# Kernel tuning notes

Hardware: AMD Instinct MI355X
Metric: run time of the kernel (lower is better)

Reference implementation:

```python
import jax, jax.numpy as jnp
import numpy as np

IN_F = 1024
OUT_F = 1024
GRID = 8
TOKENS = 8192


def setup_inputs() -> dict:
    key = jax.random.key(0)
    k_x, k_w, k_b, k_s = jax.random.split(key, 4)
    x = jax.random.normal(k_x, (TOKENS, IN_F), dtype=jnp.float32)
    # kaiming_uniform_(nonlinearity='linear'): bound = sqrt(3/fan_in)
    bound_w = float(np.sqrt(3.0 / IN_F))
    W = jax.random.uniform(k_w, (OUT_F, IN_F), minval=-bound_w, maxval=bound_w, dtype=jnp.float32)
    # nn.Linear default bias init: U(-1/sqrt(fan_in), 1/sqrt(fan_in))
    bound_b = float(1.0 / np.sqrt(IN_F))
    b = jax.random.uniform(k_b, (OUT_F,), minval=-bound_b, maxval=bound_b, dtype=jnp.float32)
    spline_weight = jax.random.uniform(k_s, (OUT_F, IN_F, GRID), minval=-0.1, maxval=0.1, dtype=jnp.float32)
    grid = jnp.linspace(-3.0, 3.0, GRID, dtype=jnp.float32)
    return {"x": x, "W": W, "b": b, "spline_weight": spline_weight, "grid": grid}


def reference(x, W, b, spline_weight, grid):
    grid_size = spline_weight.shape[-1]
    # base path: Linear(silu(x))
    base = jnp.einsum('ti,oi->to', jax.nn.silu(x), W) + b
    # RBF basis: [tokens, in_features, grid_size]
    denom = 2.0 / (grid_size - 1) + 1e-05
    basis = jnp.exp(-(((x[..., None] - grid) / denom) ** 2))
    spline = jnp.einsum('tig,oig->to', basis, spline_weight)
    return base + spline
```

## Files before the change

kernel.cpp:

```cpp
#include <hip/hip_runtime.h>
#include <hip/hip_bf16.h>

#define IN_F   1024
#define OUT_F  1024
#define TOKENS 8192
#define KTOT   9216
#define KHALF  4608
#define NTILE  72

typedef __attribute__((ext_vector_type(8))) short  bf16x8;
typedef __attribute__((ext_vector_type(8))) unsigned short ushortx8;
typedef __attribute__((ext_vector_type(4))) float  f32x4;

template<int M> struct ModeT { static constexpr int value = M; };

__device__ __forceinline__ unsigned int f2bf(float f) {
    union { float f; unsigned int u; } v; v.f = f;
    unsigned int r = v.u + 0x7fffu + ((v.u >> 16) & 1u);
    return r >> 16;
}

__device__ __forceinline__ float bf2f(unsigned short h) {
    union { unsigned int u; float f; } v; v.u = ((unsigned int)h) << 16;
    return v.f;
}

__device__ __forceinline__ void prep_a_body(int idx, const float* __restrict__ x,
                                            const float* __restrict__ grid,
                                            unsigned short* __restrict__ A)
{
    int t = idx >> 10;
    int i = idx & 1023;
    float xv = x[idx];
    float sil = xv / (1.0f + __expf(-xv));
    A[(size_t)t * KTOT + i] = (unsigned short)f2bf(sil);

    const float invd = 1.0f / (2.0f / 7.0f + 1e-5f);
    unsigned int h[8];
    #pragma unroll
    for (int g = 0; g < 8; ++g) {
        float d = (xv - grid[g]) * invd;
        h[g] = f2bf(__expf(-d * d));
    }
    uint4 pk;
    pk.x = h[0] | (h[1] << 16);
    pk.y = h[2] | (h[3] << 16);
    pk.z = h[4] | (h[5] << 16);
    pk.w = h[6] | (h[7] << 16);
    *reinterpret_cast<uint4*>(&A[(size_t)t * KTOT + IN_F + (size_t)i * 8]) = pk;
}

__device__ __forceinline__ void prep_b_body(int idx, const float* __restrict__ W,
                                            const float* __restrict__ spl,
                                            unsigned short* __restrict__ B)
{
    int o  = idx / (KTOT / 8);
    int c8 = idx - o * (KTOT / 8);
    const float* src = (c8 < IN_F / 8)
        ? (W   + (size_t)o * IN_F     + (size_t)c8 * 8)
        : (spl + (size_t)o * IN_F * 8 + (size_t)(c8 - IN_F / 8) * 8);
    const float4* s4 = reinterpret_cast<const float4*>(src);
    float4 lo = s4[0], hi = s4[1];
    uint4 pk;
    pk.x = f2bf(lo.x) | (f2bf(lo.y) << 16);
    pk.y = f2bf(lo.z) | (f2bf(lo.w) << 16);
    pk.z = f2bf(hi.x) | (f2bf(hi.y) << 16);
    pk.w = f2bf(hi.z) | (f2bf(hi.w) << 16);
    *reinterpret_cast<uint4*>(&B[(size_t)o * KTOT + (size_t)c8 * 8]) = pk;
}

__global__ __launch_bounds__(256)
void prep_fused(const float* __restrict__ x, const float* __restrict__ grid,
                const float* __restrict__ W, const float* __restrict__ spl,
                unsigned short* __restrict__ A, unsigned short* __restrict__ B)
{
    int b = blockIdx.x;
    if (b < (TOKENS * IN_F) / 256)
        prep_a_body(b * 256 + threadIdx.x, x, grid, A);
    else
        prep_b_body((b - (TOKENS * IN_F) / 256) * 256 + threadIdx.x, W, spl, B);
}

__global__ __launch_bounds__(256)
void prep_a_kernel(const float* __restrict__ x, const float* __restrict__ grid,
                   unsigned short* __restrict__ A)
{
    prep_a_body(blockIdx.x * blockDim.x + threadIdx.x, x, grid, A);
}

__global__ __launch_bounds__(256)
void prep_b_kernel(const float* __restrict__ W, const float* __restrict__ spl,
                   unsigned short* __restrict__ B)
{
    prep_b_body(blockIdx.x * blockDim.x + threadIdx.x, W, spl, B);
}

#define GLOAD(src, dst) __builtin_amdgcn_global_load_lds( \
    (const __attribute__((address_space(1))) void*)(src),  \
    (__attribute__((address_space(3))) void*)(dst), 16, 0, 0)
#define SBAR()  __builtin_amdgcn_s_barrier()
#define SCH0()  __builtin_amdgcn_sched_barrier(0)
#define VMC0()  asm volatile("s_waitcnt vmcnt(0)" ::: "memory")

__global__ __launch_bounds__(512, 2)
void gemm_kan2(const unsigned short* __restrict__ A,
               const unsigned short* __restrict__ B,
               unsigned short* __restrict__ P, int rows)
{
    __shared__ char lds[131072];

    const int bid  = blockIdx.x;
    const int xcd  = bid & 7;
    const int j    = bid >> 3;
    const int sk   = j & 1;
    const int bn   = (j >> 1) & 3;
    const int bm   = (j >> 3) * 8 + xcd;
    const int tid  = threadIdx.x;
    const int wave = tid >> 6, lane = tid & 63;
    const int wr   = wave >> 2, wc = wave & 3;
    const int fr   = lane & 15, kg = lane >> 4;
    const int sw   = fr & 7;
    const int koff[2] = { (kg ^ sw) * 16, ((4 | kg) ^ sw) * 16 };
    const int k0 = sk * KHALF;

    const int trow = tid >> 3;
    const int ksrc = ((tid & 7) ^ (trow & 7)) * 8;
    const unsigned short* gA = A + (size_t)(bm * 256 + trow) * KTOT + k0 + ksrc;
    const unsigned short* gB = B + (size_t)(bn * 256 + trow) * KTOT + k0 + ksrc;
    const size_t R64 = (size_t)64 * KTOT;

    f32x4 acc[8][4];
    const f32x4 zero = {0.f, 0.f, 0.f, 0.f};
    #pragma unroll
    for (int m = 0; m < 8; ++m)
        #pragma unroll
        for (int n = 0; n < 4; ++n) acc[m][n] = zero;

    {
        char* dA = lds + tid * 16;
        char* dB = lds + 65536 + tid * 16;
        GLOAD(gA,           dA);           GLOAD(gA + R64,     dA + 8192);
        GLOAD(gA + 2 * R64, dA + 16384);   GLOAD(gA + 3 * R64, dA + 24576);
        GLOAD(gB,           dB);           GLOAD(gB + R64,     dB + 8192);
        GLOAD(gB + 2 * R64, dB + 16384);   GLOAD(gB + 3 * R64, dB + 24576);
        gA += 64; gB += 64;
    }
    VMC0(); SBAR(); SCH0();

    const int aOff = (wr * 64 + fr) * 128;
    const int bOff = (wc * 32 + fr) * 128;

    bf16x8 af[4][2], bfLo[2][2], bfHi[2][2];
    int u = 0;

    auto tile = [&](auto mC) {
        constexpr int MODE = decltype(mC)::value;
        char* bufA = lds + (u & 1) * 32768;
        char* bufB = lds + 65536 + (u & 1) * 32768;

        #pragma unroll
        for (int mi = 0; mi < 4; ++mi)
            #pragma unroll
            for (int ks = 0; ks < 2; ++ks)
                af[mi][ks] = *(const bf16x8*)(bufA + aOff + mi * 2048 + koff[ks]);
        #pragma unroll
        for (int ni = 0; ni < 2; ++ni)
            #pragma unroll
            for (int ks = 0; ks < 2; ++ks) {
                bfLo[ni][ks] = *(const bf16x8*)(bufB + bOff + ni * 2048 + koff[ks]);
                bfHi[ni][ks] = *(const bf16x8*)(bufB + bOff + 16384 + ni * 2048 + koff[ks]);
            }

        if constexpr (MODE == 0) {
            char* dA = lds + ((u & 1) ^ 1) * 32768 + tid * 16;
            char* dB = lds + 65536 + ((u & 1) ^ 1) * 32768 + tid * 16;
            GLOAD(gA,           dA);           GLOAD(gA + R64,     dA + 8192);
            GLOAD(gA + 2 * R64, dA + 16384);   GLOAD(gA + 3 * R64, dA + 24576);
            GLOAD(gB,           dB);           GLOAD(gB + R64,     dB + 8192);
            GLOAD(gB + 2 * R64, dB + 16384);   GLOAD(gB + 3 * R64, dB + 24576);
            gA += 64; gB += 64;
        }
        SCH0();

        __builtin_amdgcn_s_setprio(1);
        #pragma unroll
        for (int mi = 0; mi < 4; ++mi)
            #pragma unroll
            for (int ni = 0; ni < 2; ++ni)
                #pragma unroll
                for (int ks = 0; ks < 2; ++ks)
                    acc[mi][ni] = __builtin_amdgcn_mfma_f32_16x16x32_bf16(
                        af[mi][ks], bfLo[ni][ks], acc[mi][ni], 0, 0, 0);
        __builtin_amdgcn_s_setprio(0);

        __builtin_amdgcn_s_setprio(1);
        #pragma unroll
        for (int mi = 0; mi < 4; ++mi)
            #pragma unroll
            for (int ni = 0; ni < 2; ++ni)
                #pragma unroll
                for (int ks = 0; ks < 2; ++ks)
                    acc[mi][2 + ni] = __builtin_amdgcn_mfma_f32_16x16x32_bf16(
                        af[mi][ks], bfHi[ni][ks], acc[mi][2 + ni], 0, 0, 0);
        __builtin_amdgcn_s_setprio(0);

        #pragma unroll
        for (int mi = 0; mi < 4; ++mi)
            #pragma unroll
            for (int ks = 0; ks < 2; ++ks)
                af[mi][ks] = *(const bf16x8*)(bufA + aOff + 16384 + mi * 2048 + koff[ks]);

        __builtin_amdgcn_s_setprio(1);
        #pragma unroll
        for (int mi = 0; mi < 4; ++mi)
            #pragma unroll
            for (int ni = 0; ni < 2; ++ni)
                #pragma unroll
                for (int ks = 0; ks < 2; ++ks)
                    acc[4 + mi][ni] = __builtin_amdgcn_mfma_f32_16x16x32_bf16(
                        af[mi][ks], bfLo[ni][ks], acc[4 + mi][ni], 0, 0, 0);
        __builtin_amdgcn_s_setprio(0);

        __builtin_amdgcn_s_setprio(1);
        #pragma unroll
        for (int mi = 0; mi < 4; ++mi)
            #pragma unroll
            for (int ni = 0; ni < 2; ++ni)
                #pragma unroll
                for (int ks = 0; ks < 2; ++ks)
                    acc[4 + mi][2 + ni] = __builtin_amdgcn_mfma_f32_16x16x32_bf16(
                        af[mi][ks], bfHi[ni][ks], acc[4 + mi][2 + ni], 0, 0, 0);
        __builtin_amdgcn_s_setprio(0);

        SCH0();
        if constexpr (MODE == 0) {
            VMC0();
            SBAR(); SCH0();
        }
    };

    for (u = 0; u < NTILE - 1; ++u) tile(ModeT<0>{});
    tile(ModeT<1>{});

    unsigned short* Pp = P + (size_t)sk * rows * OUT_F;
    const size_t orow0 = (size_t)bm * 256 + (size_t)wr * 64;
    const int    ocol0 = bn * 256 + wc * 32;
    #pragma unroll
    for (int n = 0; n < 4; ++n) {
        const int col = ocol0 + (n & 1) * 16 + (n >> 1) * 128 + fr;
        #pragma unroll
        for (int m = 0; m < 8; ++m) {
            const size_t r0 = orow0 + (m & 3) * 16 + (m >> 2) * 128 + kg * 4;
            #pragma unroll
            for (int j2 = 0; j2 < 4; ++j2)
                Pp[(r0 + j2) * OUT_F + col] = (unsigned short)f2bf(acc[m][n][j2]);
        }
    }
}

__global__ __launch_bounds__(256)
void reduce_kan(const unsigned short* __restrict__ P,
                const float* __restrict__ bias,
                float* __restrict__ out, int n8, int skStride8)
{
    const ushortx8* p0 = (const ushortx8*)P;
    const ushortx8* p1 = p0 + skStride8;
    const float4* bv = (const float4*)bias;
    float4* o = (float4*)out;
    for (int i = blockIdx.x * blockDim.x + threadIdx.x; i < n8;
         i += gridDim.x * blockDim.x) {
        ushortx8 a = p0[i], b = p1[i];
        float4 c0 = bv[(i & 127) * 2], c1 = bv[(i & 127) * 2 + 1];
        float4 r0, r1;
        r0.x = bf2f(a[0]) + bf2f(b[0]) + c0.x;
        r0.y = bf2f(a[1]) + bf2f(b[1]) + c0.y;
        r0.z = bf2f(a[2]) + bf2f(b[2]) + c0.z;
        r0.w = bf2f(a[3]) + bf2f(b[3]) + c0.w;
        r1.x = bf2f(a[4]) + bf2f(b[4]) + c1.x;
        r1.y = bf2f(a[5]) + bf2f(b[5]) + c1.y;
        r1.z = bf2f(a[6]) + bf2f(b[6]) + c1.z;
        r1.w = bf2f(a[7]) + bf2f(b[7]) + c1.w;
        o[i * 2]     = r0;
        o[i * 2 + 1] = r1;
    }
}

extern "C" void kernel_launch(void* const* d_in, const int* in_sizes, int n_in,
                              void* d_out, int out_size, void* d_ws, size_t ws_size,
                              hipStream_t stream)
{
    const float* x    = (const float*)d_in[0];
    const float* W    = (const float*)d_in[1];
    const float* bias = (const float*)d_in[2];
    const float* spl  = (const float*)d_in[3];
    const float* grid = (const float*)d_in[4];
    float* out = (float*)d_out;

    unsigned short* Bw = (unsigned short*)d_ws;
    unsigned short* Aw = Bw + (size_t)OUT_F * KTOT;

    const size_t bBytes = (size_t)OUT_F * KTOT * 2;
    size_t avail = ws_size > bBytes ? ws_size - bBytes : 0;
    long maxRows = (long)(avail / 22528);
    int chunk = (maxRows >= TOKENS) ? TOKENS : (int)((maxRows / 256) * 256);
    if (chunk < 256) chunk = 256;
    unsigned short* Pp = Aw + (size_t)chunk * KTOT;

    if (chunk == TOKENS) {
        prep_fused<<<(TOKENS * IN_F) / 256 + (OUT_F * (KTOT / 8)) / 256,
                     256, 0, stream>>>(x, grid, W, spl, Aw, Bw);
        gemm_kan2<<<(TOKENS >> 8) * 8, 512, 0, stream>>>(Aw, Bw, Pp, TOKENS);
        int n8 = TOKENS * 128;
        reduce_kan<<<2048, 256, 0, stream>>>(Pp, bias, out, n8, n8);
    } else {
        prep_b_kernel<<<(OUT_F * (KTOT / 8)) / 256, 256, 0, stream>>>(W, spl, Bw);
        for (int t0 = 0; t0 < TOKENS; t0 += chunk) {
            int rows = (TOKENS - t0 < chunk) ? (TOKENS - t0) : chunk;
            prep_a_kernel<<<(rows * IN_F) / 256, 256, 0, stream>>>(
                x + (size_t)t0 * IN_F, grid, Aw);
            gemm_kan2<<<(rows >> 8) * 8, 512, 0, stream>>>(Aw, Bw, Pp, rows);
            int n8 = rows * 128;
            int rblocks = (n8 + 255) / 256; if (rblocks > 2048) rblocks = 2048;
            reduce_kan<<<rblocks, 256, 0, stream>>>(
                Pp, bias, out + (size_t)t0 * OUT_F, n8, n8);
        }
    }
}
```

Measured before the change: 175.5 us.

## Fuse split-K reduction into GEMM epilogue via atomic counter

```diff
diff --git a/kernel.cpp b/kernel.cpp
--- a/kernel.cpp
+++ b/kernel.cpp
@@ -7,6 +7,8 @@
 #define KTOT   9216
 #define KHALF  4608
 #define NTILE  72
+#define NBA    ((TOKENS * IN_F) / 256)
+#define NBB    ((OUT_F * (KTOT / 8)) / 256)
 
 typedef __attribute__((ext_vector_type(8))) short  bf16x8;
 typedef __attribute__((ext_vector_type(8))) unsigned short ushortx8;
@@ -72,13 +74,18 @@
 __global__ __launch_bounds__(256)
 void prep_fused(const float* __restrict__ x, const float* __restrict__ grid,
                 const float* __restrict__ W, const float* __restrict__ spl,
-                unsigned short* __restrict__ A, unsigned short* __restrict__ B)
+                unsigned short* __restrict__ A, unsigned short* __restrict__ B,
+                int* __restrict__ cnt)
 {
     int b = blockIdx.x;
-    if (b < (TOKENS * IN_F) / 256)
+    if (b >= NBA + NBB) {
+        if (threadIdx.x < 128) cnt[threadIdx.x] = 0;
+        return;
+    }
+    if (b < NBA)
         prep_a_body(b * 256 + threadIdx.x, x, grid, A);
     else
-        prep_b_body((b - (TOKENS * IN_F) / 256) * 256 + threadIdx.x, W, spl, B);
+        prep_b_body((b - NBA) * 256 + threadIdx.x, W, spl, B);
 }
 
 __global__ __launch_bounds__(256)
@@ -105,7 +112,9 @@
 __global__ __launch_bounds__(512, 2)
 void gemm_kan2(const unsigned short* __restrict__ A,
                const unsigned short* __restrict__ B,
-               unsigned short* __restrict__ P, int rows)
+               unsigned short* __restrict__ P, int rows,
+               float* __restrict__ out, const float* __restrict__ bias,
+               int* __restrict__ cnt, int fuse)
 {
     __shared__ char lds[131072];
 
@@ -242,7 +251,7 @@
     for (u = 0; u < NTILE - 1; ++u) tile(ModeT<0>{});
     tile(ModeT<1>{});
 
-    unsigned short* Pp = P + (size_t)sk * rows * OUT_F;
+    unsigned short* Pown = P + (size_t)sk * rows * OUT_F;
     const size_t orow0 = (size_t)bm * 256 + (size_t)wr * 64;
     const int    ocol0 = bn * 256 + wc * 32;
     #pragma unroll
@@ -253,7 +262,32 @@
             const size_t r0 = orow0 + (m & 3) * 16 + (m >> 2) * 128 + kg * 4;
             #pragma unroll
             for (int j2 = 0; j2 < 4; ++j2)
-                Pp[(r0 + j2) * OUT_F + col] = (unsigned short)f2bf(acc[m][n][j2]);
+                Pown[(r0 + j2) * OUT_F + col] = (unsigned short)f2bf(acc[m][n][j2]);
+        }
+    }
+    if (!fuse) return;
+
+    __threadfence();
+    __syncthreads();
+    __shared__ int role;
+    if (tid == 0) role = atomicAdd(&cnt[(bm << 2) | bn], 1);
+    __syncthreads();
+    if (role == 0) return;
+    __threadfence();
+
+    const unsigned short* Poth = P + (size_t)(sk ^ 1) * rows * OUT_F;
+    #pragma unroll
+    for (int n = 0; n < 4; ++n) {
+        const int col = ocol0 + (n & 1) * 16 + (n >> 1) * 128 + fr;
+        const float bv = bias[col];
+        #pragma unroll
+        for (int m = 0; m < 8; ++m) {
+            const size_t r0 = orow0 + (m & 3) * 16 + (m >> 2) * 128 + kg * 4;
+            #pragma unroll
+            for (int j2 = 0; j2 < 4; ++j2) {
+                const size_t off = (r0 + j2) * OUT_F + col;
+                out[off] = acc[m][n][j2] + bf2f(Poth[off]) + bv;
+            }
         }
     }
 }
@@ -300,25 +334,25 @@
     unsigned short* Aw = Bw + (size_t)OUT_F * KTOT;
 
     const size_t bBytes = (size_t)OUT_F * KTOT * 2;
-    size_t avail = ws_size > bBytes ? ws_size - bBytes : 0;
+    size_t avail = ws_size > bBytes + 1024 ? ws_size - bBytes - 1024 : 0;
     long maxRows = (long)(avail / 22528);
     int chunk = (maxRows >= TOKENS) ? TOKENS : (int)((maxRows / 256) * 256);
     if (chunk < 256) chunk = 256;
     unsigned short* Pp = Aw + (size_t)chunk * KTOT;
+    int* cnt = (int*)(Pp + (size_t)2 * chunk * OUT_F);
 
     if (chunk == TOKENS) {
-        prep_fused<<<(TOKENS * IN_F) / 256 + (OUT_F * (KTOT / 8)) / 256,
-                     256, 0, stream>>>(x, grid, W, spl, Aw, Bw);
-        gemm_kan2<<<(TOKENS >> 8) * 8, 512, 0, stream>>>(Aw, Bw, Pp, TOKENS);
-        int n8 = TOKENS * 128;
-        reduce_kan<<<2048, 256, 0, stream>>>(Pp, bias, out, n8, n8);
+        prep_fused<<<NBA + NBB + 1, 256, 0, stream>>>(x, grid, W, spl, Aw, Bw, cnt);
+        gemm_kan2<<<(TOKENS >> 8) * 8, 512, 0, stream>>>(
+            Aw, Bw, Pp, TOKENS, out, bias, cnt, 1);
     } else {
-        prep_b_kernel<<<(OUT_F * (KTOT / 8)) / 256, 256, 0, stream>>>(W, spl, Bw);
+        prep_b_kernel<<<NBB, 256, 0, stream>>>(W, spl, Bw);
         for (int t0 = 0; t0 < TOKENS; t0 += chunk) {
             int rows = (TOKENS - t0 < chunk) ? (TOKENS - t0) : chunk;
             prep_a_kernel<<<(rows * IN_F) / 256, 256, 0, stream>>>(
                 x + (size_t)t0 * IN_F, grid, Aw);
-            gemm_kan2<<<(rows >> 8) * 8, 512, 0, stream>>>(Aw, Bw, Pp, rows);
+            gemm_kan2<<<(rows >> 8) * 8, 512, 0, stream>>>(
+                Aw, Bw, Pp, rows, out + (size_t)t0 * OUT_F, bias, cnt, 0);
             int n8 = rows * 128;
             int rblocks = (n8 + 255) / 256; if (rblocks > 2048) rblocks = 2048;
             reduce_kan<<<rblocks, 256, 0, stream>>>(
```

After: 281.9 us. 60.6% more time.

## Shrink GEMM block tile to 128x128 with 4 waves and halved LDS

Applied to the files above, without the earlier changes.

```diff
diff --git a/kernel.cpp b/kernel.cpp
--- a/kernel.cpp
+++ b/kernel.cpp
@@ -7,6 +7,8 @@
 #define KTOT   9216
 #define KHALF  4608
 #define NTILE  72
+#define NBA    ((TOKENS * IN_F) / 256)
+#define NBB    ((OUT_F * (KTOT / 8)) / 256)
 
 typedef __attribute__((ext_vector_type(8))) short  bf16x8;
 typedef __attribute__((ext_vector_type(8))) unsigned short ushortx8;
@@ -75,10 +77,10 @@
                 unsigned short* __restrict__ A, unsigned short* __restrict__ B)
 {
     int b = blockIdx.x;
-    if (b < (TOKENS * IN_F) / 256)
+    if (b < NBA)
         prep_a_body(b * 256 + threadIdx.x, x, grid, A);
     else
-        prep_b_body((b - (TOKENS * IN_F) / 256) * 256 + threadIdx.x, W, spl, B);
+        prep_b_body((b - NBA) * 256 + threadIdx.x, W, spl, B);
 }
 
 __global__ __launch_bounds__(256)
@@ -102,22 +104,22 @@
 #define SCH0()  __builtin_amdgcn_sched_barrier(0)
 #define VMC0()  asm volatile("s_waitcnt vmcnt(0)" ::: "memory")
 
-__global__ __launch_bounds__(512, 2)
+__global__ __launch_bounds__(256, 2)
 void gemm_kan2(const unsigned short* __restrict__ A,
                const unsigned short* __restrict__ B,
                unsigned short* __restrict__ P, int rows)
 {
-    __shared__ char lds[131072];
+    __shared__ char lds[65536];
 
     const int bid  = blockIdx.x;
     const int xcd  = bid & 7;
     const int j    = bid >> 3;
     const int sk   = j & 1;
-    const int bn   = (j >> 1) & 3;
-    const int bm   = (j >> 3) * 8 + xcd;
+    const int bn   = (j >> 1) & 7;
+    const int bm   = (j >> 4) * 8 + xcd;
     const int tid  = threadIdx.x;
     const int wave = tid >> 6, lane = tid & 63;
-    const int wr   = wave >> 2, wc = wave & 3;
+    const int wr   = wave >> 1, wc = wave & 1;
     const int fr   = lane & 15, kg = lane >> 4;
     const int sw   = fr & 7;
     const int koff[2] = { (kg ^ sw) * 16, ((4 | kg) ^ sw) * 16 };
@@ -125,59 +127,56 @@
 
     const int trow = tid >> 3;
     const int ksrc = ((tid & 7) ^ (trow & 7)) * 8;
-    const unsigned short* gA = A + (size_t)(bm * 256 + trow) * KTOT + k0 + ksrc;
-    const unsigned short* gB = B + (size_t)(bn * 256 + trow) * KTOT + k0 + ksrc;
-    const size_t R64 = (size_t)64 * KTOT;
-
-    f32x4 acc[8][4];
+    const unsigned short* gA = A + (size_t)(bm * 128 + trow) * KTOT + k0 + ksrc;
+    const unsigned short* gB = B + (size_t)(bn * 128 + trow) * KTOT + k0 + ksrc;
+    const size_t R32 = (size_t)32 * KTOT;
+
+    f32x4 acc[4][4];
     const f32x4 zero = {0.f, 0.f, 0.f, 0.f};
     #pragma unroll
-    for (int m = 0; m < 8; ++m)
+    for (int m = 0; m < 4; ++m)
         #pragma unroll
         for (int n = 0; n < 4; ++n) acc[m][n] = zero;
 
     {
         char* dA = lds + tid * 16;
-        char* dB = lds + 65536 + tid * 16;
-        GLOAD(gA,           dA);           GLOAD(gA + R64,     dA + 8192);
-        GLOAD(gA + 2 * R64, dA + 16384);   GLOAD(gA + 3 * R64, dA + 24576);
-        GLOAD(gB,           dB);           GLOAD(gB + R64,     dB + 8192);
-        GLOAD(gB + 2 * R64, dB + 16384);   GLOAD(gB + 3 * R64, dB + 24576);
+        char* dB = lds + 32768 + tid * 16;
+        #pragma unroll
+        for (int r = 0; r < 4; ++r) {
+            GLOAD(gA + r * R32, dA + r * 4096);
+            GLOAD(gB + r * R32, dB + r * 4096);
+        }
         gA += 64; gB += 64;
     }
     VMC0(); SBAR(); SCH0();
 
     const int aOff = (wr * 64 + fr) * 128;
-    const int bOff = (wc * 32 + fr) * 128;
-
-    bf16x8 af[4][2], bfLo[2][2], bfHi[2][2];
+    const int bOff = (wc * 64 + fr) * 128;
+
+    bf16x8 af[4][2], bf[4][2];
     int u = 0;
 
     auto tile = [&](auto mC) {
         constexpr int MODE = decltype(mC)::value;
-        char* bufA = lds + (u & 1) * 32768;
-        char* bufB = lds + 65536 + (u & 1) * 32768;
+        char* bufA = lds + (u & 1) * 16384;
+        char* bufB = lds + 32768 + (u & 1) * 16384;
 
         #pragma unroll
         for (int mi = 0; mi < 4; ++mi)
             #pragma unroll
-            for (int ks = 0; ks < 2; ++ks)
+            for (int ks = 0; ks < 2; ++ks) {
                 af[mi][ks] = *(const bf16x8*)(bufA + aOff + mi * 2048 + koff[ks]);
-        #pragma unroll
-        for (int ni = 0; ni < 2; ++ni)
-            #pragma unroll
-            for (int ks = 0; ks < 2; ++ks) {
-                bfLo[ni][ks] = *(const bf16x8*)(bufB + bOff + ni * 2048 + koff[ks]);
-                bfHi[ni][ks] = *(const bf16x8*)(bufB + bOff + 16384 + ni * 2048 + koff[ks]);
+                bf[mi][ks] = *(const bf16x8*)(bufB + bOff + mi * 2048 + koff[ks]);
             }
 
         if constexpr (MODE == 0) {
-            char* dA = lds + ((u & 1) ^ 1) * 32768 + tid * 16;
-            char* dB = lds + 65536 + ((u & 1) ^ 1) * 32768 + tid * 16;
-            GLOAD(gA,           dA);           GLOAD(gA + R64,     dA + 8192);
-            GLOAD(gA + 2 * R64, dA + 16384);   GLOAD(gA + 3 * R64, dA + 24576);
-            GLOAD(gB,           dB);           GLOAD(gB + R64,     dB + 8192);
-            GLOAD(gB + 2 * R64, dB + 16384);   GLOAD(gB + 3 * R64, dB + 24576);
+            char* dA = lds + ((u & 1) ^ 1) * 16384 + tid * 16;
+            char* dB = lds + 32768 + ((u & 1) ^ 1) * 16384 + tid * 16;
+            #pragma unroll
+            for (int r = 0; r < 4; ++r) {
+                GLOAD(gA + r * R32, dA + r * 4096);
+                GLOAD(gB + r * R32, dB + r * 4096);
+            }
             gA += 64; gB += 64;
         }
         SCH0();
@@ -186,50 +185,11 @@
         #pragma unroll
         for (int mi = 0; mi < 4; ++mi)
             #pragma unroll
-            for (int ni = 0; ni < 2; ++ni)
+            for (int ni = 0; ni < 4; ++ni)
                 #pragma unroll
                 for (int ks = 0; ks < 2; ++ks)
                     acc[mi][ni] = __builtin_amdgcn_mfma_f32_16x16x32_bf16(
-                        af[mi][ks], bfLo[ni][ks], acc[mi][ni], 0, 0, 0);
-        __builtin_amdgcn_s_setprio(0);
-
-        __builtin_amdgcn_s_setprio(1);
-        #pragma unroll
-        for (int mi = 0; mi < 4; ++mi)
-            #pragma unroll
-            for (int ni = 0; ni < 2; ++ni)
-                #pragma unroll
-                for (int ks = 0; ks < 2; ++ks)
-                    acc[mi][2 + ni] = __builtin_amdgcn_mfma_f32_16x16x32_bf16(
-                        af[mi][ks], bfHi[ni][ks], acc[mi][2 + ni], 0, 0, 0);
-        __builtin_amdgcn_s_setprio(0);
-
-        #pragma unroll
-        for (int mi = 0; mi < 4; ++mi)
-            #pragma unroll
-            for (int ks = 0; ks < 2; ++ks)
-                af[mi][ks] = *(const bf16x8*)(bufA + aOff + 16384 + mi * 2048 + koff[ks]);
-
-        __builtin_amdgcn_s_setprio(1);
-        #pragma unroll
-        for (int mi = 0; mi < 4; ++mi)
-            #pragma unroll
-            for (int ni = 0; ni < 2; ++ni)
-                #pragma unroll
-                for (int ks = 0; ks < 2; ++ks)
-                    acc[4 + mi][ni] = __builtin_amdgcn_mfma_f32_16x16x32_bf16(
-                        af[mi][ks], bfLo[ni][ks], acc[4 + mi][ni], 0, 0, 0);
-        __builtin_amdgcn_s_setprio(0);
-
-        __builtin_amdgcn_s_setprio(1);
-        #pragma unroll
-        for (int mi = 0; mi < 4; ++mi)
-            #pragma unroll
-            for (int ni = 0; ni < 2; ++ni)
-                #pragma unroll
-                for (int ks = 0; ks < 2; ++ks)
-                    acc[4 + mi][2 + ni] = __builtin_amdgcn_mfma_f32_16x16x32_bf16(
-                        af[mi][ks], bfHi[ni][ks], acc[4 + mi][2 + ni], 0, 0, 0);
+                        af[mi][ks], bf[ni][ks], acc[mi][ni], 0, 0, 0);
         __builtin_amdgcn_s_setprio(0);
 
         SCH0();
@@ -243,14 +203,14 @@
     tile(ModeT<1>{});
 
     unsigned short* Pp = P + (size_t)sk * rows * OUT_F;
-    const size_t orow0 = (size_t)bm * 256 + (size_t)wr * 64;
-    const int    ocol0 = bn * 256 + wc * 32;
+    const size_t orow0 = (size_t)bm * 128 + (size_t)wr * 64;
+    const int    ocol0 = bn * 128 + wc * 64;
     #pragma unroll
     for (int n = 0; n < 4; ++n) {
-        const int col = ocol0 + (n & 1) * 16 + (n >> 1) * 128 + fr;
-        #pragma unroll
-        for (int m = 0; m < 8; ++m) {
-            const size_t r0 = orow0 + (m & 3) * 16 + (m >> 2) * 128 + kg * 4;
+        const int col = ocol0 + n * 16 + fr;
+        #pragma unroll
+        for (int m = 0; m < 4; ++m) {
+            const size_t r0 = orow0 + m * 16 + kg * 4;
             #pragma unroll
             for (int j2 = 0; j2 < 4; ++j2)
                 Pp[(r0 + j2) * OUT_F + col] = (unsigned short)f2bf(acc[m][n][j2]);
@@ -302,23 +262,22 @@
     const size_t bBytes = (size_t)OUT_F * KTOT * 2;
     size_t avail = ws_size > bBytes ? ws_size - bBytes : 0;
     long maxRows = (long)(avail / 22528);
-    int chunk = (maxRows >= TOKENS) ? TOKENS : (int)((maxRows / 256) * 256);
-    if (chunk < 256) chunk = 256;
+    int chunk = (maxRows >= TOKENS) ? TOKENS : (int)((maxRows / 1024) * 1024);
+    if (chunk < 1024) chunk = 1024;
     unsigned short* Pp = Aw + (size_t)chunk * KTOT;
 
     if (chunk == TOKENS) {
-        prep_fused<<<(TOKENS * IN_F) / 256 + (OUT_F * (KTOT / 8)) / 256,
-                     256, 0, stream>>>(x, grid, W, spl, Aw, Bw);
-        gemm_kan2<<<(TOKENS >> 8) * 8, 512, 0, stream>>>(Aw, Bw, Pp, TOKENS);
+        prep_fused<<<NBA + NBB, 256, 0, stream>>>(x, grid, W, spl, Aw, Bw);
+        gemm_kan2<<<(TOKENS >> 7) * 16, 256, 0, stream>>>(Aw, Bw, Pp, TOKENS);
         int n8 = TOKENS * 128;
         reduce_kan<<<2048, 256, 0, stream>>>(Pp, bias, out, n8, n8);
     } else {
-        prep_b_kernel<<<(OUT_F * (KTOT / 8)) / 256, 256, 0, stream>>>(W, spl, Bw);
+        prep_b_kernel<<<NBB, 256, 0, stream>>>(W, spl, Bw);
         for (int t0 = 0; t0 < TOKENS; t0 += chunk) {
             int rows = (TOKENS - t0 < chunk) ? (TOKENS - t0) : chunk;
             prep_a_kernel<<<(rows * IN_F) / 256, 256, 0, stream>>>(
                 x + (size_t)t0 * IN_F, grid, Aw);
-            gemm_kan2<<<(rows >> 8) * 8, 512, 0, stream>>>(Aw, Bw, Pp, rows);
+            gemm_kan2<<<(rows >> 7) * 16, 256, 0, stream>>>(Aw, Bw, Pp, rows);
             int n8 = rows * 128;
             int rblocks = (n8 + 255) / 256; if (rblocks > 2048) rblocks = 2048;
             reduce_kan<<<rblocks, 256, 0, stream>>>(
```

After: 194.8 us. 11.0% more time.
